# Performance work log

Measured on AMD Instinct MI355X. Metric: run time of the kernel, lower is better.

Reference implementation:

```python
import jax, jax.numpy as jnp
import numpy as np

B, H, Wd, C = 8, 64, 64, 128
KH, KW = 3, 3
N = KH * KW  # kernel_n
F = 256


def _grid_offset(h, w, kh, kw):
    """Replicates the TensorLayer grid construction exactly, including the
    (2,kh,kw)->(kh*kw,2) reshape of the stacked meshgrid."""
    n = kh * kw
    initial = np.stack(np.meshgrid(np.arange(kh), np.arange(kw), indexing='ij'))  # (2,kh,kw)
    initial = initial.reshape(-1, 2).astype(np.float32)  # (n,2), faithful flattening order
    gy = np.arange(-int((kh - 1) / 2.0), h - int((kh - 1) / 2.0))
    gx = np.arange(-int((kw - 1) / 2.0), w - int((kw - 1) / 2.0))
    grid = np.stack(np.meshgrid(gy, gx, indexing='ij'), axis=-1).astype(np.float32)  # (h,w,2)
    grid = np.tile(grid[:, :, None, :], (1, 1, n, 1))  # (h,w,n,2)
    return jnp.asarray(grid + initial[None, None, :, :])  # (h,w,n,2)


def setup_inputs() -> dict:
    key = jax.random.key(0)
    k1, k2, k3 = jax.random.split(key, 3)
    x = jax.random.normal(k1, (B, H, Wd, C), dtype=jnp.float32)
    offsets = jax.random.normal(k2, (B, H, Wd, 2 * N), dtype=jnp.float32)
    W = jax.random.normal(k3, (N, C, F), dtype=jnp.float32) * 0.02  # truncated_normal(0.02) analogue
    b = jnp.zeros((F,), dtype=jnp.float32)
    return {"x": x, "offsets": offsets, "W": W, "b": b}


def reference(x, offsets, W, b):
    h, w = x.shape[1], x.shape[2]
    grid = _grid_offset(h, w, KH, KW)  # (h,w,n,2)
    coords = grid[None] + offsets.reshape(x.shape[0], h, w, N, 2)  # (b,h,w,n,2)
    cy = jnp.clip(coords[..., 0], 0.0, jnp.float32(h - 1))
    cx = jnp.clip(coords[..., 1], 0.0, jnp.float32(w - 1))
    y0 = jnp.floor(cy).astype(jnp.int32)
    y1 = jnp.ceil(cy).astype(jnp.int32)
    x0 = jnp.floor(cx).astype(jnp.int32)
    x1 = jnp.ceil(cx).astype(jnp.int32)

    bidx = jnp.arange(x.shape[0])[:, None, None, None]

    def gather(yy, xx):
        return x[bidx, yy, xx]  # (b,h,w,n,c)

    v_lt = gather(y0, x0)
    v_rb = gather(y1, x1)
    v_lb = gather(y0, x1)  # (lt_y, rb_x) as in original
    v_rt = gather(y1, x0)  # (rb_y, lt_x) as in original

    fy = (cy - y0.astype(cy.dtype))[..., None]
    fx = (cx - x0.astype(cx.dtype))[..., None]
    vals_t = v_lt + (v_rt - v_lt) * fy
    vals_b = v_lb + (v_rb - v_lb) * fy
    mapped = vals_t + (vals_b - vals_t) * fx  # (b,h,w,n,c)

    # conv3d with kernel [1,1,n,c,f] + VALID == contraction over (n,c)
    out = jnp.einsum('bhwnc,ncf->bhwf', mapped, W) + b
    return out
```

## Files before the change

### kernel.cpp

```cpp
#include <hip/hip_runtime.h>

#define HH 64
#define WW 64
#define CC 128
#define FF 256
#define NTAP 9
#define KD 1152
#define XELEMS (8 * HH * WW * CC)
#define XCVT_BLOCKS (XELEMS / (256 * 8))
#define WT_BLOCKS 144

typedef __attribute__((ext_vector_type(8))) short bf16x8;
typedef __attribute__((ext_vector_type(4))) float floatx4;

__device__ inline unsigned short f2bf(float v) {
  union { float f; unsigned u; } c; c.f = v;
  unsigned r = (c.u + 0x7FFFu + ((c.u >> 16) & 1u)) >> 16;
  return (unsigned short)r;
}
__device__ inline float bflo(unsigned u) {
  union { unsigned u; float f; } c; c.u = u << 16; return c.f;
}
__device__ inline float bfhi(unsigned u) {
  union { unsigned u; float f; } c; c.u = u & 0xFFFF0000u; return c.f;
}
__device__ inline unsigned cvt_pk_bf16(float lo, float hi) {
  unsigned r;
  asm("v_cvt_pk_bf16_f32 %0, %1, %2" : "=v"(r) : "v"(lo), "v"(hi));
  return r;
}

#define IY_PACK 0x18690
#define IX_PACK 0x21894

struct ITap { int b00, b10, b01, b11; float w00, w10, w01, w11; };

__device__ inline ITap tap_from(float2 o2, int i, int p, int n) {
  float cy = (float)(i - 1 + ((IY_PACK >> (2 * n)) & 3)) + o2.x;
  float cx = (float)(p - 1 + ((IX_PACK >> (2 * n)) & 3)) + o2.y;
  cy = fminf(fmaxf(cy, 0.f), 63.f);
  cx = fminf(fmaxf(cx, 0.f), 63.f);
  const float fy0 = floorf(cy), fx0 = floorf(cx);
  const int y0 = (int)fy0, y1 = (int)ceilf(cy);
  const int x0 = (int)fx0, x1 = (int)ceilf(cx);
  const float fy = cy - fy0, fx = cx - fx0;
  const float gy0 = 1.f - fy, gx0 = 1.f - fx;
  ITap t;
  t.b00 = (y0 * WW + x0) * CC;
  t.b10 = (y1 * WW + x0) * CC;
  t.b01 = (y0 * WW + x1) * CC;
  t.b11 = (y1 * WW + x1) * CC;
  t.w00 = gy0 * gx0;
  t.w10 = fy  * gx0;
  t.w01 = gy0 * fx;
  t.w11 = fy  * fx;
  return t;
}

__device__ inline unsigned lerp_word(unsigned u00, unsigned u10, unsigned u01, unsigned u11,
                                     const ITap& t) {
  float rlo = bflo(u00) * t.w00 + bflo(u10) * t.w10 + bflo(u01) * t.w01 + bflo(u11) * t.w11;
  float rhi = bfhi(u00) * t.w00 + bfhi(u10) * t.w10 + bfhi(u01) * t.w01 + bfhi(u11) * t.w11;
  return cvt_pk_bf16(rlo, rhi);
}

__global__ void prep_kernel(const float* __restrict__ X, const float* __restrict__ W,
                            unsigned short* __restrict__ Xb, unsigned short* __restrict__ Wt) {
  const int blk = blockIdx.x;
  if (blk < XCVT_BLOCKS) {
    const int t = blk * 256 + threadIdx.x;
    const float4* src = (const float4*)(X + (size_t)t * 8);
    float4 a = src[0], b2 = src[1];
    bf16x8 o;
    o[0] = (short)f2bf(a.x);  o[1] = (short)f2bf(a.y);
    o[2] = (short)f2bf(a.z);  o[3] = (short)f2bf(a.w);
    o[4] = (short)f2bf(b2.x); o[5] = (short)f2bf(b2.y);
    o[6] = (short)f2bf(b2.z); o[7] = (short)f2bf(b2.w);
    *(bf16x8*)(Xb + (size_t)t * 8) = o;
  } else {
    const int t = (blk - XCVT_BLOCKS) * 256 + threadIdx.x;
    const int f = t & 255;
    const int k0 = (t >> 8) * 8;
    unsigned short o[8];
#pragma unroll
    for (int i2 = 0; i2 < 8; ++i2)
      o[i2] = f2bf(W[(size_t)(k0 + i2) * FF + f]);
    *(uint4*)(Wt + (size_t)f * KD + k0) = *(uint4*)o;
  }
}

__global__ __launch_bounds__(512, 4) void fused_kernel(
    const unsigned short* __restrict__ Xb, const float* __restrict__ Off,
    const unsigned short* __restrict__ Wt, const float* __restrict__ bias,
    float* __restrict__ Out)
{
  __shared__ unsigned short smA[2][64 * 64];
  __shared__ unsigned short smB[2][256 * 64];

  const int blk = blockIdx.x;
  const int b   = blk & 7;
  const int i   = blk >> 3;
  const int m0  = (b * 64 + i) * 64;
  const int tid = threadIdx.x;
  const int wave = tid >> 6, lane = tid & 63;
  const int wm   = (wave & 1) * 32;
  const int wf   = (wave >> 1) * 64;
  const int arow = lane & 15, aq = lane >> 4;
  const int p  = tid >> 3;
  const int c0 = tid & 7;

  const unsigned short* xb = Xb + (size_t)b * (HH * WW * CC);
  const float* offp = Off + ((size_t)(b * HH + i) * WW + p) * (2 * NTAP);

  floatx4 acc[2][4];
#pragma unroll
  for (int mt = 0; mt < 2; ++mt)
#pragma unroll
    for (int ft = 0; ft < 4; ++ft)
      acc[mt][ft] = (floatx4){0.f, 0.f, 0.f, 0.f};

#define STAGE_B(KT, BUF)                                                             \
  {                                                                                  \
    _Pragma("unroll")                                                                \
    for (int pass = 0; pass < 4; ++pass) {                                           \
      const int row = pass * 64 + (tid >> 3);                                        \
      const int chp = c0 ^ (row & 7);                                                \
      const unsigned short* gp = Wt + (size_t)row * KD + (KT) * 64 + chp * 8;        \
      unsigned short* l = (unsigned short*)&smB[BUF][row * 64 + c0 * 8];             \
      __builtin_amdgcn_global_load_lds(                                              \
          (const __attribute__((address_space(1))) unsigned int*)gp,                 \
          (__attribute__((address_space(3))) unsigned int*)l, 16, 0, 0);             \
    }                                                                                \
  }

  ITap t = tap_from(*(const float2*)offp, i, p, 0);
  STAGE_B(0, 0)
  {
    const int ch = c0 * 8;
    uint4 q00 = *(const uint4*)(xb + t.b00 + ch);
    uint4 q10 = *(const uint4*)(xb + t.b10 + ch);
    uint4 q01 = *(const uint4*)(xb + t.b01 + ch);
    uint4 q11 = *(const uint4*)(xb + t.b11 + ch);
    unsigned w0 = lerp_word(q00.x, q10.x, q01.x, q11.x, t);
    unsigned w1 = lerp_word(q00.y, q10.y, q01.y, q11.y, t);
    unsigned w2 = lerp_word(q00.z, q10.z, q01.z, q11.z, t);
    unsigned w3 = lerp_word(q00.w, q10.w, q01.w, q11.w, t);
    *(uint4*)&smA[0][p * 64 + ((c0 ^ (p & 7)) << 3)] = make_uint4(w0, w1, w2, w3);
  }
  __syncthreads();

  int cur = 0;
  for (int kt = 0; kt < 18; ++kt) {
    bf16x8 afr[2][2], bfr[2][4];
#pragma unroll
    for (int ks = 0; ks < 2; ++ks) {
      const int slot = (((ks * 4 + aq) ^ (arow & 7)) << 3);
#pragma unroll
      for (int mt = 0; mt < 2; ++mt)
        afr[ks][mt] = *(const bf16x8*)&smA[cur][(wm + mt * 16 + arow) * 64 + slot];
#pragma unroll
      for (int ft = 0; ft < 4; ++ft)
        bfr[ks][ft] = *(const bf16x8*)&smB[cur][(wf + ft * 16 + arow) * 64 + slot];
    }

    const int nk = kt + 1;
    uint4 g0, g1, g2, g3;
    if (nk < 18) {
      if ((nk & 1) == 0)
        t = tap_from(*(const float2*)(offp + 2 * (nk >> 1)), i, p, nk >> 1);
      const int ch = ((nk & 1) * 8 + c0) * 8;
      g0 = *(const uint4*)(xb + t.b00 + ch);
      g1 = *(const uint4*)(xb + t.b10 + ch);
      g2 = *(const uint4*)(xb + t.b01 + ch);
      g3 = *(const uint4*)(xb + t.b11 + ch);
      STAGE_B(nk, cur ^ 1)
    }

#pragma unroll
    for (int ks = 0; ks < 2; ++ks)
#pragma unroll
      for (int mt = 0; mt < 2; ++mt)
#pragma unroll
        for (int ft = 0; ft < 4; ++ft)
          acc[mt][ft] = __builtin_amdgcn_mfma_f32_16x16x32_bf16(
              afr[ks][mt], bfr[ks][ft], acc[mt][ft], 0, 0, 0);

    if (nk < 18) {
      unsigned w0 = lerp_word(g0.x, g1.x, g2.x, g3.x, t);
      unsigned w1 = lerp_word(g0.y, g1.y, g2.y, g3.y, t);
      unsigned w2 = lerp_word(g0.z, g1.z, g2.z, g3.z, t);
      unsigned w3 = lerp_word(g0.w, g1.w, g2.w, g3.w, t);
      *(uint4*)&smA[cur ^ 1][p * 64 + ((c0 ^ (p & 7)) << 3)] = make_uint4(w0, w1, w2, w3);
    }
    __syncthreads();
    cur ^= 1;
  }
#undef STAGE_B

  float bv[4];
#pragma unroll
  for (int ft = 0; ft < 4; ++ft)
    bv[ft] = bias[wf + ft * 16 + arow];
#pragma unroll
  for (int mt = 0; mt < 2; ++mt) {
#pragma unroll
    for (int ft = 0; ft < 4; ++ft) {
      const int f = wf + ft * 16 + arow;
#pragma unroll
      for (int r = 0; r < 4; ++r) {
        const int m = m0 + wm + mt * 16 + aq * 4 + r;
        Out[(size_t)m * FF + f] = acc[mt][ft][r] + bv[ft];
      }
    }
  }
}

extern "C" void kernel_launch(void* const* d_in, const int* in_sizes, int n_in,
                              void* d_out, int out_size, void* d_ws, size_t ws_size,
                              hipStream_t stream) {
  const float* X    = (const float*)d_in[0];
  const float* Off  = (const float*)d_in[1];
  const float* W    = (const float*)d_in[2];
  const float* bias = (const float*)d_in[3];
  float* Out = (float*)d_out;

  unsigned short* Wt = (unsigned short*)d_ws;
  unsigned short* Xb = Wt + (size_t)FF * KD;

  prep_kernel<<<XCVT_BLOCKS + WT_BLOCKS, 256, 0, stream>>>(X, W, Xb, Wt);
  fused_kernel<<<512, 512, 0, stream>>>(Xb, Off, Wt, bias, Out);
}
```

Before: 112.4 us.

## Pre-swizzle weights into MFMA fragment order and read B directly from global

The weight prep kernel now writes W in the exact per-lane MFMA fragment layout, so the fused kernel loads B fragments straight from global or L2 into registers and no longer stages them in LDS. Blocks shrink to 256 threads covering 32 output pixels, with each wave owning 64 output features, and the grid doubles to 1024 blocks. The gather for the next tap is issued a full iteration ahead, giving a deeper software pipeline. This removes LDS traffic and the large smB buffer, which should help occupancy. In exchange every block re-reads the whole weight matrix from global memory, and each A tile feeds fewer MFMAs.

```diff
diff --git a/kernel.cpp b/kernel.cpp
--- a/kernel.cpp
+++ b/kernel.cpp
@@ -30,42 +30,38 @@
   return r;
 }
 
+__device__ inline unsigned lerp_word(unsigned u00, unsigned u10, unsigned u01, unsigned u11,
+                                     float w00, float w10, float w01, float w11) {
+  float rlo = bflo(u00) * w00 + bflo(u10) * w10 + bflo(u01) * w01 + bflo(u11) * w11;
+  float rhi = bfhi(u00) * w00 + bfhi(u10) * w10 + bfhi(u01) * w01 + bfhi(u11) * w11;
+  return cvt_pk_bf16(rlo, rhi);
+}
+
 #define IY_PACK 0x18690
 #define IX_PACK 0x21894
 
-struct ITap { int b00, b10, b01, b11; float w00, w10, w01, w11; };
-
-__device__ inline ITap tap_from(float2 o2, int i, int p, int n) {
-  float cy = (float)(i - 1 + ((IY_PACK >> (2 * n)) & 3)) + o2.x;
-  float cx = (float)(p - 1 + ((IX_PACK >> (2 * n)) & 3)) + o2.y;
+struct ITap { int b00, b10, b01, b11; float fy, fx; };
+
+__device__ inline ITap tap_from(float2 o2, int yy, int xx, int n) {
+  float cy = (float)(yy - 1 + ((IY_PACK >> (2 * n)) & 3)) + o2.x;
+  float cx = (float)(xx - 1 + ((IX_PACK >> (2 * n)) & 3)) + o2.y;
   cy = fminf(fmaxf(cy, 0.f), 63.f);
   cx = fminf(fmaxf(cx, 0.f), 63.f);
   const float fy0 = floorf(cy), fx0 = floorf(cx);
   const int y0 = (int)fy0, y1 = (int)ceilf(cy);
   const int x0 = (int)fx0, x1 = (int)ceilf(cx);
-  const float fy = cy - fy0, fx = cx - fx0;
-  const float gy0 = 1.f - fy, gx0 = 1.f - fx;
   ITap t;
   t.b00 = (y0 * WW + x0) * CC;
   t.b10 = (y1 * WW + x0) * CC;
   t.b01 = (y0 * WW + x1) * CC;
   t.b11 = (y1 * WW + x1) * CC;
-  t.w00 = gy0 * gx0;
-  t.w10 = fy  * gx0;
-  t.w01 = gy0 * fx;
-  t.w11 = fy  * fx;
+  t.fy = cy - fy0;
+  t.fx = cx - fx0;
   return t;
 }
 
-__device__ inline unsigned lerp_word(unsigned u00, unsigned u10, unsigned u01, unsigned u11,
-                                     const ITap& t) {
-  float rlo = bflo(u00) * t.w00 + bflo(u10) * t.w10 + bflo(u01) * t.w01 + bflo(u11) * t.w11;
-  float rhi = bfhi(u00) * t.w00 + bfhi(u10) * t.w10 + bfhi(u01) * t.w01 + bfhi(u11) * t.w11;
-  return cvt_pk_bf16(rlo, rhi);
-}
-
 __global__ void prep_kernel(const float* __restrict__ X, const float* __restrict__ W,
-                            unsigned short* __restrict__ Xb, unsigned short* __restrict__ Wt) {
+                            unsigned short* __restrict__ Xb, unsigned short* __restrict__ Wtf) {
   const int blk = blockIdx.x;
   if (blk < XCVT_BLOCKS) {
     const int t = blk * 256 + threadIdx.x;
@@ -79,38 +75,41 @@
     *(bf16x8*)(Xb + (size_t)t * 8) = o;
   } else {
     const int t = (blk - XCVT_BLOCKS) * 256 + threadIdx.x;
-    const int f = t & 255;
-    const int k0 = (t >> 8) * 8;
+    const int f  = t & 255;
+    const int kc = t >> 8;
     unsigned short o[8];
 #pragma unroll
-    for (int i2 = 0; i2 < 8; ++i2)
-      o[i2] = f2bf(W[(size_t)(k0 + i2) * FF + f]);
-    *(uint4*)(Wt + (size_t)f * KD + k0) = *(uint4*)o;
-  }
-}
-
-__global__ __launch_bounds__(512, 4) void fused_kernel(
+    for (int j = 0; j < 8; ++j)
+      o[j] = f2bf(W[(size_t)(kc * 8 + j) * FF + f]);
+    const int kt = kc >> 3, ks = (kc >> 2) & 1, aq = kc & 3;
+    const int fg = f >> 6, ft = (f >> 4) & 3, arow = f & 15;
+    const size_t addr = (size_t)((kt * 2 + ks) * 16 + fg * 4 + ft) * 512 + aq * 128 + arow * 8;
+    *(uint4*)(Wtf + addr) = *(uint4*)o;
+  }
+}
+
+__global__ __launch_bounds__(256, 4) void fused_kernel(
     const unsigned short* __restrict__ Xb, const float* __restrict__ Off,
-    const unsigned short* __restrict__ Wt, const float* __restrict__ bias,
+    const unsigned short* __restrict__ Wtf, const float* __restrict__ bias,
     float* __restrict__ Out)
 {
-  __shared__ unsigned short smA[2][64 * 64];
-  __shared__ unsigned short smB[2][256 * 64];
+  __shared__ unsigned short smA[2][32 * 64];
 
   const int blk = blockIdx.x;
   const int b   = blk & 7;
   const int i   = blk >> 3;
-  const int m0  = (b * 64 + i) * 64;
+  const int y   = i >> 1;
+  const int m0  = b * 4096 + i * 32;
   const int tid = threadIdx.x;
   const int wave = tid >> 6, lane = tid & 63;
-  const int wm   = (wave & 1) * 32;
-  const int wf   = (wave >> 1) * 64;
   const int arow = lane & 15, aq = lane >> 4;
-  const int p  = tid >> 3;
-  const int c0 = tid & 7;
-
-  const unsigned short* xb = Xb + (size_t)b * (HH * WW * CC);
-  const float* offp = Off + ((size_t)(b * HH + i) * WW + p) * (2 * NTAP);
+  const int p   = tid >> 3;
+  const int c0  = tid & 7;
+  const int px  = (i & 1) * 32 + p;
+
+  const unsigned short* xb   = Xb + (size_t)b * (HH * WW * CC);
+  const float* offp          = Off + ((size_t)(b * HH + y) * WW + px) * (2 * NTAP);
+  const unsigned short* wbase = Wtf + (size_t)wave * 2048 + (size_t)lane * 8;
 
   floatx4 acc[2][4];
 #pragma unroll
@@ -119,96 +118,106 @@
     for (int ft = 0; ft < 4; ++ft)
       acc[mt][ft] = (floatx4){0.f, 0.f, 0.f, 0.f};
 
-#define STAGE_B(KT, BUF)                                                             \
-  {                                                                                  \
-    _Pragma("unroll")                                                                \
-    for (int pass = 0; pass < 4; ++pass) {                                           \
-      const int row = pass * 64 + (tid >> 3);                                        \
-      const int chp = c0 ^ (row & 7);                                                \
-      const unsigned short* gp = Wt + (size_t)row * KD + (KT) * 64 + chp * 8;        \
-      unsigned short* l = (unsigned short*)&smB[BUF][row * 64 + c0 * 8];             \
-      __builtin_amdgcn_global_load_lds(                                              \
-          (const __attribute__((address_space(1))) unsigned int*)gp,                 \
-          (__attribute__((address_space(3))) unsigned int*)l, 16, 0, 0);             \
-    }                                                                                \
-  }
-
-  ITap t = tap_from(*(const float2*)offp, i, p, 0);
-  STAGE_B(0, 0)
+  const int sa_off = p * 64 + ((c0 ^ (p & 7)) << 3);
+
+  ITap tL = tap_from(*(const float2*)offp, y, px, 0);
+  uint4 g0, g1, g2, g3;
   {
     const int ch = c0 * 8;
-    uint4 q00 = *(const uint4*)(xb + t.b00 + ch);
-    uint4 q10 = *(const uint4*)(xb + t.b10 + ch);
-    uint4 q01 = *(const uint4*)(xb + t.b01 + ch);
-    uint4 q11 = *(const uint4*)(xb + t.b11 + ch);
-    unsigned w0 = lerp_word(q00.x, q10.x, q01.x, q11.x, t);
-    unsigned w1 = lerp_word(q00.y, q10.y, q01.y, q11.y, t);
-    unsigned w2 = lerp_word(q00.z, q10.z, q01.z, q11.z, t);
-    unsigned w3 = lerp_word(q00.w, q10.w, q01.w, q11.w, t);
-    *(uint4*)&smA[0][p * 64 + ((c0 ^ (p & 7)) << 3)] = make_uint4(w0, w1, w2, w3);
-  }
+    uint4 q00 = *(const uint4*)(xb + tL.b00 + ch);
+    uint4 q10 = *(const uint4*)(xb + tL.b10 + ch);
+    uint4 q01 = *(const uint4*)(xb + tL.b01 + ch);
+    uint4 q11 = *(const uint4*)(xb + tL.b11 + ch);
+    const float gy = 1.f - tL.fy, gx = 1.f - tL.fx;
+    const float w00 = gy * gx, w10 = tL.fy * gx, w01 = gy * tL.fx, w11 = tL.fy * tL.fx;
+    uint4 o;
+    o.x = lerp_word(q00.x, q10.x, q01.x, q11.x, w00, w10, w01, w11);
+    o.y = lerp_word(q00.y, q10.y, q01.y, q11.y, w00, w10, w01, w11);
+    o.z = lerp_word(q00.z, q10.z, q01.z, q11.z, w00, w10, w01, w11);
+    o.w = lerp_word(q00.w, q10.w, q01.w, q11.w, w00, w10, w01, w11);
+    *(uint4*)&smA[0][sa_off] = o;
+    const int ch1 = (8 + c0) * 8;
+    g0 = *(const uint4*)(xb + tL.b00 + ch1);
+    g1 = *(const uint4*)(xb + tL.b10 + ch1);
+    g2 = *(const uint4*)(xb + tL.b01 + ch1);
+    g3 = *(const uint4*)(xb + tL.b11 + ch1);
+  }
+  ITap tG = tL;
   __syncthreads();
 
   int cur = 0;
   for (int kt = 0; kt < 18; ++kt) {
-    bf16x8 afr[2][2], bfr[2][4];
+    const unsigned short* wk = wbase + (size_t)kt * 16384;
+
+    bf16x8 b0[4], b1[4];
+#pragma unroll
+    for (int ft = 0; ft < 4; ++ft)
+      b0[ft] = *(const bf16x8*)(wk + ft * 512);
+
+    bf16x8 afr[2][2];
 #pragma unroll
     for (int ks = 0; ks < 2; ++ks) {
       const int slot = (((ks * 4 + aq) ^ (arow & 7)) << 3);
 #pragma unroll
       for (int mt = 0; mt < 2; ++mt)
-        afr[ks][mt] = *(const bf16x8*)&smA[cur][(wm + mt * 16 + arow) * 64 + slot];
+        afr[ks][mt] = *(const bf16x8*)&smA[cur][(mt * 16 + arow) * 64 + slot];
+    }
+
+    if (kt <= 16) {
+      const float gy = 1.f - tL.fy, gx = 1.f - tL.fx;
+      const float w00 = gy * gx, w10 = tL.fy * gx, w01 = gy * tL.fx, w11 = tL.fy * tL.fx;
+      uint4 o;
+      o.x = lerp_word(g0.x, g1.x, g2.x, g3.x, w00, w10, w01, w11);
+      o.y = lerp_word(g0.y, g1.y, g2.y, g3.y, w00, w10, w01, w11);
+      o.z = lerp_word(g0.z, g1.z, g2.z, g3.z, w00, w10, w01, w11);
+      o.w = lerp_word(g0.w, g1.w, g2.w, g3.w, w00, w10, w01, w11);
+      *(uint4*)&smA[cur ^ 1][sa_off] = o;
+    }
+
+#pragma unroll
+    for (int ft = 0; ft < 4; ++ft)
+      b1[ft] = *(const bf16x8*)(wk + 8192 + ft * 512);
+
+    if (kt <= 15) {
+      if ((kt & 1) == 0)
+        tG = tap_from(*(const float2*)(offp + 2 * ((kt + 2) >> 1)), y, px, (kt + 2) >> 1);
+      const int ch = ((kt & 1) * 8 + c0) * 8;
+      g0 = *(const uint4*)(xb + tG.b00 + ch);
+      g1 = *(const uint4*)(xb + tG.b10 + ch);
+      g2 = *(const uint4*)(xb + tG.b01 + ch);
+      g3 = *(const uint4*)(xb + tG.b11 + ch);
+    }
+
+#pragma unroll
+    for (int mt = 0; mt < 2; ++mt)
 #pragma unroll
       for (int ft = 0; ft < 4; ++ft)
-        bfr[ks][ft] = *(const bf16x8*)&smB[cur][(wf + ft * 16 + arow) * 64 + slot];
-    }
-
-    const int nk = kt + 1;
-    uint4 g0, g1, g2, g3;
-    if (nk < 18) {
-      if ((nk & 1) == 0)
-        t = tap_from(*(const float2*)(offp + 2 * (nk >> 1)), i, p, nk >> 1);
-      const int ch = ((nk & 1) * 8 + c0) * 8;
-      g0 = *(const uint4*)(xb + t.b00 + ch);
-      g1 = *(const uint4*)(xb + t.b10 + ch);
-      g2 = *(const uint4*)(xb + t.b01 + ch);
-      g3 = *(const uint4*)(xb + t.b11 + ch);
-      STAGE_B(nk, cur ^ 1)
-    }
-
-#pragma unroll
-    for (int ks = 0; ks < 2; ++ks)
-#pragma unroll
-      for (int mt = 0; mt < 2; ++mt)
-#pragma unroll
-        for (int ft = 0; ft < 4; ++ft)
-          acc[mt][ft] = __builtin_amdgcn_mfma_f32_16x16x32_bf16(
-              afr[ks][mt], bfr[ks][ft], acc[mt][ft], 0, 0, 0);
-
-    if (nk < 18) {
-      unsigned w0 = lerp_word(g0.x, g1.x, g2.x, g3.x, t);
-      unsigned w1 = lerp_word(g0.y, g1.y, g2.y, g3.y, t);
-      unsigned w2 = lerp_word(g0.z, g1.z, g2.z, g3.z, t);
-      unsigned w3 = lerp_word(g0.w, g1.w, g2.w, g3.w, t);
-      *(uint4*)&smA[cur ^ 1][p * 64 + ((c0 ^ (p & 7)) << 3)] = make_uint4(w0, w1, w2, w3);
-    }
+        acc[mt][ft] = __builtin_amdgcn_mfma_f32_16x16x32_bf16(
+            afr[0][mt], b0[ft], acc[mt][ft], 0, 0, 0);
+#pragma unroll
+    for (int mt = 0; mt < 2; ++mt)
+#pragma unroll
+      for (int ft = 0; ft < 4; ++ft)
+        acc[mt][ft] = __builtin_amdgcn_mfma_f32_16x16x32_bf16(
+            afr[1][mt], b1[ft], acc[mt][ft], 0, 0, 0);
+
     __syncthreads();
     cur ^= 1;
-  }
-#undef STAGE_B
+    tL = tG;
+  }
 
   float bv[4];
 #pragma unroll
   for (int ft = 0; ft < 4; ++ft)
-    bv[ft] = bias[wf + ft * 16 + arow];
+    bv[ft] = bias[wave * 64 + ft * 16 + arow];
 #pragma unroll
   for (int mt = 0; mt < 2; ++mt) {
 #pragma unroll
     for (int ft = 0; ft < 4; ++ft) {
-      const int f = wf + ft * 16 + arow;
+      const int f = wave * 64 + ft * 16 + arow;
 #pragma unroll
       for (int r = 0; r < 4; ++r) {
-        const int m = m0 + wm + mt * 16 + aq * 4 + r;
+        const int m = m0 + mt * 16 + aq * 4 + r;
         Out[(size_t)m * FF + f] = acc[mt][ft][r] + bv[ft];
       }
     }
@@ -224,9 +233,9 @@
   const float* bias = (const float*)d_in[3];
   float* Out = (float*)d_out;
 
-  unsigned short* Wt = (unsigned short*)d_ws;
-  unsigned short* Xb = Wt + (size_t)FF * KD;
-
-  prep_kernel<<<XCVT_BLOCKS + WT_BLOCKS, 256, 0, stream>>>(X, W, Xb, Wt);
-  fused_kernel<<<512, 512, 0, stream>>>(Xb, Off, Wt, bias, Out);
-}
+  unsigned short* Wtf = (unsigned short*)d_ws;
+  unsigned short* Xb  = Wtf + (size_t)FF * KD;
+
+  prep_kernel<<<XCVT_BLOCKS + WT_BLOCKS, 256, 0, stream>>>(X, W, Xb, Wtf);
+  fused_kernel<<<1024, 256, 0, stream>>>(Xb, Off, Wtf, bias, Out);
+}
```

Result: faster. 110.1 us (-2.0%).
